# Optimization experiments

Hardware: AMD Instinct MI355X
Metric: run time of the kernel (lower is better)

The kernel has to match this reference:

```python
import jax, jax.numpy as jnp
import numpy as np

# Bit-slice configuration from the module defaults: slices [1,1,2,4] -> 8-bit signed INT.
# The crossbar engine's MapReduceDot decomposes the quantized integers into bit-planes,
# runs partial dot products per (input-slice, weight-slice) pair across paral_size
# partitions, and recombines them with 2^shift weights. In the ideal (noise-free)
# engine this recombination is EXACT, so the forward math equals:
#   dequant(blockwise_quant(x)) @ dequant(blockwise_quant(W^T)) + bias
# with per-block scales determined by the quant granularities.
IN_BITS = 1 + 1 + 2 + 4   # sum(input_slice)  = 8
W_BITS = 1 + 1 + 2 + 4    # sum(weight_slice) = 8
IN_GRAN = (1, 32)         # (rows, cols) blocks over (seq, in_features)
W_GRAN = (32, 32)         # blocks over (in_features, out_features) of weight.t()


def block_fake_quant(x, bits, gran):
    """Symmetric per-block fake quantization (quantize -> dequantize).

    x: [..., R, C]; gran=(gr, gc) tiles the last two dims. Each (gr, gc) block
    gets its own max-abs scale, matching SlicedData's quant_gran semantics.
    """
    qmax = float(2 ** (bits - 1) - 1)  # 127 for 8-bit
    gr, gc = gran
    lead = x.shape[:-2]
    R, C = x.shape[-2], x.shape[-1]
    xb = x.reshape(*lead, R // gr, gr, C // gc, gc)
    mx = jnp.max(jnp.abs(xb), axis=(-3, -1), keepdims=True)
    scale = jnp.where(mx > 0, mx / qmax, jnp.ones_like(mx))
    q = jnp.clip(jnp.round(xb / scale), -qmax, qmax) * scale
    return q.reshape(x.shape)


def setup_inputs() -> dict:
    key = jax.random.key(0)
    k1, k2, k3 = jax.random.split(key, 3)
    B, S, Din, Dout = 4, 4096, 2048, 2048
    x = jax.random.normal(k1, (B, S, Din), dtype=jnp.float32)
    # kaiming_uniform_(a=sqrt(5)) on a Linear weight is U(-1/sqrt(fan_in), 1/sqrt(fan_in))
    bound = 1.0 / np.sqrt(Din)
    weight = jax.random.uniform(k2, (Dout, Din), jnp.float32, -bound, bound)
    bias = jax.random.uniform(k3, (Dout,), jnp.float32, -bound, bound)
    return {"x": x, "weight": weight, "bias": bias}


def reference(x, weight, bias):
    # Quantize activations per (1, 32) block and weight.t() per (32, 32) block,
    # then recombine via the (mathematically exact) bit-sliced dot == dense GEMM
    # on the dequantized values.
    qx = block_fake_quant(x, IN_BITS, IN_GRAN)            # [B, S, Din]
    qw = block_fake_quant(weight.T, W_BITS, W_GRAN)       # [Din, Dout]
    out = jnp.einsum('bsd,de->bse', qx, qw) + bias        # [B, S, Dout]
    return out
```

## Files before the change

### kernel.cpp

```cpp
#include <hip/hip_runtime.h>
#include <hip/hip_bf16.h>
#include <stdint.h>

#define M_TOT 16384
#define N_TOT 2048
#define K_TOT 2048
#define NT 32

typedef __attribute__((ext_vector_type(8))) short bf16x8;
typedef __attribute__((ext_vector_type(4))) float f32x4;

__device__ __forceinline__ ushort f32_to_bf16_rne(float f) {
    uint32_t u = __float_as_uint(f);
    uint32_t r = (u + 0x7fffu + ((u >> 16) & 1u)) >> 16;
    return (ushort)r;
}

__device__ __forceinline__ void async_copy16(const void* gptr, void* lptr) {
    __builtin_amdgcn_global_load_lds(
        (const __attribute__((address_space(1))) uint32_t*)gptr,
        (__attribute__((address_space(3))) uint32_t*)lptr,
        16, 0, 0);
}

__global__ void quant_x_kernel(const float* __restrict__ x, ushort* __restrict__ qx) {
    const int tid = blockIdx.x * 256 + threadIdx.x;
    const float4 v = ((const float4*)x)[tid];
    float m = fmaxf(fmaxf(fabsf(v.x), fabsf(v.y)), fmaxf(fabsf(v.z), fabsf(v.w)));
    m = fmaxf(m, __shfl_xor(m, 1));
    m = fmaxf(m, __shfl_xor(m, 2));
    m = fmaxf(m, __shfl_xor(m, 4));
    const float s = (m > 0.f) ? (m / 127.f) : 1.f;
    const float q0 = fminf(fmaxf(rintf(v.x / s), -127.f), 127.f) * s;
    const float q1 = fminf(fmaxf(rintf(v.y / s), -127.f), 127.f) * s;
    const float q2 = fminf(fmaxf(rintf(v.z / s), -127.f), 127.f) * s;
    const float q3 = fminf(fmaxf(rintf(v.w / s), -127.f), 127.f) * s;
    ushort4 r;
    r.x = f32_to_bf16_rne(q0);
    r.y = f32_to_bf16_rne(q1);
    r.z = f32_to_bf16_rne(q2);
    r.w = f32_to_bf16_rne(q3);
    ((ushort4*)qx)[tid] = r;
}

__global__ void quant_w_kernel(const float* __restrict__ w, ushort* __restrict__ qw) {
    const int gtid = blockIdx.x * 256 + threadIdx.x;
    const int wid  = gtid >> 6;
    const int lane = gtid & 63;
    const int tn = wid >> 6;
    const int tk = wid & 63;
    const int row = tn * 32 + (lane >> 1);
    const int col = tk * 32 + ((lane & 1) << 4);
    const float* p = w + (size_t)row * K_TOT + col;
    const float4 v0 = ((const float4*)p)[0];
    const float4 v1 = ((const float4*)p)[1];
    const float4 v2 = ((const float4*)p)[2];
    const float4 v3 = ((const float4*)p)[3];
    float m = 0.f;
#define MAX4(V) m = fmaxf(m, fmaxf(fmaxf(fabsf(V.x), fabsf(V.y)), fmaxf(fabsf(V.z), fabsf(V.w))));
    MAX4(v0) MAX4(v1) MAX4(v2) MAX4(v3)
#undef MAX4
    #pragma unroll
    for (int off = 1; off < 64; off <<= 1) m = fmaxf(m, __shfl_xor(m, off));
    const float s = (m > 0.f) ? (m / 127.f) : 1.f;
    float vv[16] = {v0.x, v0.y, v0.z, v0.w, v1.x, v1.y, v1.z, v1.w,
                    v2.x, v2.y, v2.z, v2.w, v3.x, v3.y, v3.z, v3.w};
    union { ushort us[16]; uint4 q[2]; } o;
    #pragma unroll
    for (int i = 0; i < 16; ++i) {
        const float q = fminf(fmaxf(rintf(vv[i] / s), -127.f), 127.f) * s;
        o.us[i] = f32_to_bf16_rne(q);
    }
    uint4* dst = (uint4*)(qw + (size_t)row * K_TOT + col);
    dst[0] = o.q[0];
    dst[1] = o.q[1];
}

#define LDSA(tb, row, colus) \
    (*(const bf16x8*)&As[tb][row][(colus) ^ (((row) & 7) << 3)])
#define LDSB(tb, row, colus) \
    (*(const bf16x8*)&Bs[tb][row][(colus) ^ (((row) & 7) << 3)])

#define STAGE_A(tb, hh, li, tt)                                                          \
    async_copy16(Agbase + (size_t)((hh) * 128 + (li) * 64) * K_TOT + (size_t)(tt) * 64,  \
                 (char*)&As[0][0][0] + (tb) * 32768 + (hh) * 16384 + (li) * 8192 + (wv << 10))
#define STAGE_B(tb, hh, li, tt)                                                          \
    async_copy16(Bgbase + (size_t)((hh) * 128 + (li) * 64) * K_TOT + (size_t)(tt) * 64,  \
                 (char*)&Bs[0][0][0] + (tb) * 32768 + (hh) * 16384 + (li) * 8192 + (wv << 10))
#define STAGE_A2(tb, hh, tt)  { STAGE_A(tb, hh, 0, tt); STAGE_A(tb, hh, 1, tt); }
#define STAGE_B2(tb, hh, tt)  { STAGE_B(tb, hh, 0, tt); STAGE_B(tb, hh, 1, tt); }

#define PHASE_MFMA(i0)                                                                    \
    asm volatile("s_waitcnt lgkmcnt(0)" ::: "memory");                                    \
    __builtin_amdgcn_s_setprio(1);                                                        \
    _Pragma("unroll")                                                                     \
    for (int j = 0; j < 4; ++j) {                                                         \
        acc[i0][j]     = __builtin_amdgcn_mfma_f32_16x16x32_bf16(af0, bg[j][0], acc[i0][j], 0, 0, 0);     \
        acc[i0][j]     = __builtin_amdgcn_mfma_f32_16x16x32_bf16(af1, bg[j][1], acc[i0][j], 0, 0, 0);     \
        acc[(i0)+1][j] = __builtin_amdgcn_mfma_f32_16x16x32_bf16(af2, bg[j][0], acc[(i0)+1][j], 0, 0, 0); \
        acc[(i0)+1][j] = __builtin_amdgcn_mfma_f32_16x16x32_bf16(af3, bg[j][1], acc[(i0)+1][j], 0, 0, 0); \
    }                                                                                     \
    __builtin_amdgcn_s_setprio(0);

#define TILE_BODY(tb, t)                                                                  \
  {                                                                                       \
    bf16x8 af0, af1, af2, af3;                                                            \
    bf16x8 bg[4][2];                                                                      \
                      \
    af0 = LDSA(tb, ab +  0, h8);  af1 = LDSA(tb, ab +  0, 32 + h8);                       \
    af2 = LDSA(tb, ab + 16, h8);  af3 = LDSA(tb, ab + 16, 32 + h8);                       \
    bg[0][0] = LDSB(tb, bb0, h8);  bg[0][1] = LDSB(tb, bb0, 32 + h8);                     \
    bg[1][0] = LDSB(tb, bb1, h8);  bg[1][1] = LDSB(tb, bb1, 32 + h8);                     \
    bg[2][0] = LDSB(tb, bb2, h8);  bg[2][1] = LDSB(tb, bb2, 32 + h8);                     \
    bg[3][0] = LDSB(tb, bb3, h8);  bg[3][1] = LDSB(tb, bb3, 32 + h8);                     \
    if ((t) + 1 < NT) STAGE_A2(tb ^ 1, 0, (t) + 1)                                        \
    asm volatile("s_waitcnt lgkmcnt(8)" ::: "memory");                                    \
    __builtin_amdgcn_s_barrier();                                                         \
    PHASE_MFMA(0)                                                                         \
    __builtin_amdgcn_s_barrier();                                                         \
                                \
    af0 = LDSA(tb, ab + 32, h8);  af1 = LDSA(tb, ab + 32, 32 + h8);                       \
    af2 = LDSA(tb, ab + 48, h8);  af3 = LDSA(tb, ab + 48, 32 + h8);                       \
    if ((t) + 1 < NT) STAGE_A2(tb ^ 1, 1, (t) + 1)                                        \
    __builtin_amdgcn_s_barrier();                                                         \
    PHASE_MFMA(2)                                                                         \
    __builtin_amdgcn_s_barrier();                                                         \
           \
    af0 = LDSA(tb, ab + 64, h8);  af1 = LDSA(tb, ab + 64, 32 + h8);                       \
    af2 = LDSA(tb, ab + 80, h8);  af3 = LDSA(tb, ab + 80, 32 + h8);                       \
    if ((t) + 2 < NT) STAGE_B2(tb, 0, (t) + 2)                                            \
    __builtin_amdgcn_s_barrier();                                                         \
    PHASE_MFMA(4)                                                                         \
    __builtin_amdgcn_s_barrier();                                                         \
                \
    af0 = LDSA(tb, ab +  96, h8);  af1 = LDSA(tb, ab +  96, 32 + h8);                     \
    af2 = LDSA(tb, ab + 112, h8);  af3 = LDSA(tb, ab + 112, 32 + h8);                     \
    if ((t) + 2 < NT) STAGE_B2(tb, 1, (t) + 2)                                            \
    __builtin_amdgcn_s_barrier();                                                         \
    PHASE_MFMA(6)                                                                         \
    if ((t) + 2 < NT) { asm volatile("s_waitcnt vmcnt(4)" ::: "memory"); }                \
    else              { asm volatile("s_waitcnt vmcnt(0)" ::: "memory"); }                \
    __builtin_amdgcn_s_barrier();                                                         \
  }

__global__ __launch_bounds__(512, 1) void gemm_8ph_kernel(
    const ushort* __restrict__ A,
    const ushort* __restrict__ Bt,
    const float* __restrict__ bias,
    float* __restrict__ C) {

    __shared__ ushort As[2][256][64];
    __shared__ ushort Bs[2][256][64];

    const int tid  = threadIdx.x;
    const int lane = tid & 63;
    const int wv   = tid >> 6;
    const int wmr  = wv >> 2;
    const int wcn  = wv & 3;
    const int r    = lane & 15;
    const int h8   = (lane >> 4) << 3;

    const int nbn  = N_TOT / 256;
    const int nwg  = (M_TOT / 256) * nbn;
    const int cpx  = nwg >> 3;
    const int swz  = (blockIdx.x & 7) * cpx + (blockIdx.x >> 3);
    const int brow = (swz / nbn) * 256;
    const int bcol = (swz % nbn) * 256;

    const int srow = tid >> 3;
    const int scol = (((tid & 7) ^ (srow & 7)) << 3);
    const ushort* Agbase = A  + (size_t)(brow + srow) * K_TOT + scol;
    const ushort* Bgbase = Bt + (size_t)(bcol + srow) * K_TOT + scol;

    const int ab  = wmr * 128 + r;
    const int bb0 = wcn * 64 +  0 + r;
    const int bb1 = wcn * 64 + 16 + r;
    const int bb2 = wcn * 64 + 32 + r;
    const int bb3 = wcn * 64 + 48 + r;

    f32x4 acc[8][4];
    const f32x4 zero = {0.f, 0.f, 0.f, 0.f};
    #pragma unroll
    for (int i = 0; i < 8; ++i)
        #pragma unroll
        for (int j = 0; j < 4; ++j) acc[i][j] = zero;

    STAGE_A2(0, 0, 0) STAGE_A2(0, 1, 0)
    STAGE_B2(0, 0, 0) STAGE_B2(0, 1, 0)
    STAGE_B2(1, 0, 1) STAGE_B2(1, 1, 1)
    asm volatile("s_waitcnt vmcnt(4)" ::: "memory");
    __builtin_amdgcn_s_barrier();

    for (int t = 0; t < NT; t += 2) {
        TILE_BODY(0, t)
        TILE_BODY(1, t + 1)
    }

    const int hq = (lane >> 4) * 4;
    float bv[4];
    #pragma unroll
    for (int j = 0; j < 4; ++j) bv[j] = bias[bcol + wcn * 64 + j * 16 + r];
    #pragma unroll
    for (int i = 0; i < 8; ++i) {
        const int row0 = brow + wmr * 128 + i * 16 + hq;
        #pragma unroll
        for (int j = 0; j < 4; ++j) {
            const int col = bcol + wcn * 64 + j * 16 + r;
            #pragma unroll
            for (int jj = 0; jj < 4; ++jj)
                C[(size_t)(row0 + jj) * N_TOT + col] = acc[i][j][jj] + bv[j];
        }
    }
}

extern "C" void kernel_launch(void* const* d_in, const int* in_sizes, int n_in,
                              void* d_out, int out_size, void* d_ws, size_t ws_size,
                              hipStream_t stream) {
    const float* x    = (const float*)d_in[0];
    const float* wgt  = (const float*)d_in[1];
    const float* bias = (const float*)d_in[2];
    float* out = (float*)d_out;

    ushort* qx = (ushort*)d_ws;
    ushort* qw = qx + (size_t)M_TOT * K_TOT;

    quant_x_kernel<<<(M_TOT * K_TOT / 4) / 256, 256, 0, stream>>>(x, qx);
    quant_w_kernel<<<(64 * 64 * 64) / 256, 256, 0, stream>>>(wgt, qw);
    gemm_8ph_kernel<<<(M_TOT / 256) * (N_TOT / 256), 512, 0, stream>>>(qx, qw, bias, out);
}
```

Before: 175.3 us.

## Ping-pong A fragments in registers and drop most per-phase barriers in GEMM loop

Restructures the GEMM main loop so A fragments are double-buffered in two register sets (afX/afY). The LDS read for the next phase is issued before the current phase's MFMAs, using partial lgkmcnt waits and sched_barriers. Block-wide barriers drop from eight per K-tile to two, and the last two tiles are peeled to remove per-iteration staging conditionals. It also changes launch_bounds to request two 512-thread blocks per CU. That cap likely squeezes registers against the 128-float accumulator and may cause spills, while the LDS footprint per block probably prevents two blocks from co-residing anyway.

```diff
diff --git a/kernel.cpp b/kernel.cpp
--- a/kernel.cpp
+++ b/kernel.cpp
@@ -83,67 +83,69 @@
 
 #define STAGE_A(tb, hh, li, tt)                                                          \
     async_copy16(Agbase + (size_t)((hh) * 128 + (li) * 64) * K_TOT + (size_t)(tt) * 64,  \
-                 (char*)&As[0][0][0] + (tb) * 32768 + (hh) * 16384 + (li) * 8192 + (wv << 10))
+                 (char*)&As[0][0][0] + (tb) * 32768 + (hh) * 16384 + (li) * 8192 + (wv << 10));
 #define STAGE_B(tb, hh, li, tt)                                                          \
     async_copy16(Bgbase + (size_t)((hh) * 128 + (li) * 64) * K_TOT + (size_t)(tt) * 64,  \
-                 (char*)&Bs[0][0][0] + (tb) * 32768 + (hh) * 16384 + (li) * 8192 + (wv << 10))
-#define STAGE_A2(tb, hh, tt)  { STAGE_A(tb, hh, 0, tt); STAGE_A(tb, hh, 1, tt); }
-#define STAGE_B2(tb, hh, tt)  { STAGE_B(tb, hh, 0, tt); STAGE_B(tb, hh, 1, tt); }
-
-#define PHASE_MFMA(i0)                                                                    \
-    asm volatile("s_waitcnt lgkmcnt(0)" ::: "memory");                                    \
+                 (char*)&Bs[0][0][0] + (tb) * 32768 + (hh) * 16384 + (li) * 8192 + (wv << 10));
+#define STAGE_A2(tb, hh, tt)  { STAGE_A(tb, hh, 0, tt) STAGE_A(tb, hh, 1, tt) }
+#define STAGE_B2(tb, hh, tt)  { STAGE_B(tb, hh, 0, tt) STAGE_B(tb, hh, 1, tt) }
+
+#define WAITLGKM4 { asm volatile("s_waitcnt lgkmcnt(4)" ::: "memory"); __builtin_amdgcn_sched_barrier(0); }
+#define WAITLGKM0 { asm volatile("s_waitcnt lgkmcnt(0)" ::: "memory"); __builtin_amdgcn_sched_barrier(0); }
+#define WAITVM4   { asm volatile("s_waitcnt vmcnt(4)" ::: "memory"); }
+#define WAITVM0   { asm volatile("s_waitcnt vmcnt(0)" ::: "memory"); }
+
+#define RD_AF(DST, tb, q) {                                   \
+    DST[0] = LDSA(tb, ab + (q) * 32,      h8);                \
+    DST[1] = LDSA(tb, ab + (q) * 32,      32 + h8);           \
+    DST[2] = LDSA(tb, ab + (q) * 32 + 16, h8);                \
+    DST[3] = LDSA(tb, ab + (q) * 32 + 16, 32 + h8); }
+
+#define MFMA_PH(i0, AF)                                                                   \
     __builtin_amdgcn_s_setprio(1);                                                        \
     _Pragma("unroll")                                                                     \
     for (int j = 0; j < 4; ++j) {                                                         \
-        acc[i0][j]     = __builtin_amdgcn_mfma_f32_16x16x32_bf16(af0, bg[j][0], acc[i0][j], 0, 0, 0);     \
-        acc[i0][j]     = __builtin_amdgcn_mfma_f32_16x16x32_bf16(af1, bg[j][1], acc[i0][j], 0, 0, 0);     \
-        acc[(i0)+1][j] = __builtin_amdgcn_mfma_f32_16x16x32_bf16(af2, bg[j][0], acc[(i0)+1][j], 0, 0, 0); \
-        acc[(i0)+1][j] = __builtin_amdgcn_mfma_f32_16x16x32_bf16(af3, bg[j][1], acc[(i0)+1][j], 0, 0, 0); \
+        acc[i0][j]     = __builtin_amdgcn_mfma_f32_16x16x32_bf16(AF[0], bg[j][0], acc[i0][j], 0, 0, 0);     \
+        acc[i0][j]     = __builtin_amdgcn_mfma_f32_16x16x32_bf16(AF[1], bg[j][1], acc[i0][j], 0, 0, 0);     \
+        acc[(i0)+1][j] = __builtin_amdgcn_mfma_f32_16x16x32_bf16(AF[2], bg[j][0], acc[(i0)+1][j], 0, 0, 0); \
+        acc[(i0)+1][j] = __builtin_amdgcn_mfma_f32_16x16x32_bf16(AF[3], bg[j][1], acc[(i0)+1][j], 0, 0, 0); \
     }                                                                                     \
     __builtin_amdgcn_s_setprio(0);
 
-#define TILE_BODY(tb, t)                                                                  \
+#define TILE_BODY(tb, t, STA, STB, VMC)                                                   \
   {                                                                                       \
-    bf16x8 af0, af1, af2, af3;                                                            \
-    bf16x8 bg[4][2];                                                                      \
-                      \
-    af0 = LDSA(tb, ab +  0, h8);  af1 = LDSA(tb, ab +  0, 32 + h8);                       \
-    af2 = LDSA(tb, ab + 16, h8);  af3 = LDSA(tb, ab + 16, 32 + h8);                       \
-    bg[0][0] = LDSB(tb, bb0, h8);  bg[0][1] = LDSB(tb, bb0, 32 + h8);                     \
-    bg[1][0] = LDSB(tb, bb1, h8);  bg[1][1] = LDSB(tb, bb1, 32 + h8);                     \
-    bg[2][0] = LDSB(tb, bb2, h8);  bg[2][1] = LDSB(tb, bb2, 32 + h8);                     \
-    bg[3][0] = LDSB(tb, bb3, h8);  bg[3][1] = LDSB(tb, bb3, 32 + h8);                     \
-    if ((t) + 1 < NT) STAGE_A2(tb ^ 1, 0, (t) + 1)                                        \
-    asm volatile("s_waitcnt lgkmcnt(8)" ::: "memory");                                    \
-    __builtin_amdgcn_s_barrier();                                                         \
-    PHASE_MFMA(0)                                                                         \
-    __builtin_amdgcn_s_barrier();                                                         \
-                                \
-    af0 = LDSA(tb, ab + 32, h8);  af1 = LDSA(tb, ab + 32, 32 + h8);                       \
-    af2 = LDSA(tb, ab + 48, h8);  af3 = LDSA(tb, ab + 48, 32 + h8);                       \
-    if ((t) + 1 < NT) STAGE_A2(tb ^ 1, 1, (t) + 1)                                        \
-    __builtin_amdgcn_s_barrier();                                                         \
-    PHASE_MFMA(2)                                                                         \
-    __builtin_amdgcn_s_barrier();                                                         \
-           \
-    af0 = LDSA(tb, ab + 64, h8);  af1 = LDSA(tb, ab + 64, 32 + h8);                       \
-    af2 = LDSA(tb, ab + 80, h8);  af3 = LDSA(tb, ab + 80, 32 + h8);                       \
-    if ((t) + 2 < NT) STAGE_B2(tb, 0, (t) + 2)                                            \
-    __builtin_amdgcn_s_barrier();                                                         \
-    PHASE_MFMA(4)                                                                         \
-    __builtin_amdgcn_s_barrier();                                                         \
-                \
-    af0 = LDSA(tb, ab +  96, h8);  af1 = LDSA(tb, ab +  96, 32 + h8);                     \
-    af2 = LDSA(tb, ab + 112, h8);  af3 = LDSA(tb, ab + 112, 32 + h8);                     \
-    if ((t) + 2 < NT) STAGE_B2(tb, 1, (t) + 2)                                            \
-    __builtin_amdgcn_s_barrier();                                                         \
-    PHASE_MFMA(6)                                                                         \
-    if ((t) + 2 < NT) { asm volatile("s_waitcnt vmcnt(4)" ::: "memory"); }                \
-    else              { asm volatile("s_waitcnt vmcnt(0)" ::: "memory"); }                \
-    __builtin_amdgcn_s_barrier();                                                         \
+               \
+    RD_AF(afX, tb, 0)                                                                     \
+    _Pragma("unroll")                                                                     \
+    for (int j = 0; j < 4; ++j) {                                                         \
+        const int bb = wcn * 64 + j * 16 + r;                                             \
+        bg[j][0] = LDSB(tb, bb, h8);  bg[j][1] = LDSB(tb, bb, 32 + h8);                   \
+    }                                                                                     \
+    RD_AF(afY, tb, 1)                                                                     \
+    if (STA) STAGE_A2(tb ^ 1, 0, (t) + 1)                                                 \
+    WAITLGKM4                                                                             \
+    MFMA_PH(0, afX)                                                                       \
+                                 \
+    RD_AF(afX, tb, 2)                                                                     \
+    if (STA) STAGE_A2(tb ^ 1, 1, (t) + 1)                                                 \
+    WAITLGKM4                                                                             \
+    MFMA_PH(2, afY)                                                                       \
+    __builtin_amdgcn_s_barrier();                \
+                                 \
+    RD_AF(afY, tb, 3)                                                                     \
+    if (STB) STAGE_B2(tb, 0, (t) + 2)                                                     \
+    WAITLGKM4                                                                             \
+    MFMA_PH(4, afX)                                                                       \
+                       \
+    if (STB) STAGE_B2(tb, 1, (t) + 2)                                                     \
+    WAITLGKM0                                                                             \
+    MFMA_PH(6, afY)                                                                       \
+    if ((VMC) == 4)      WAITVM4                                                          \
+    else if ((VMC) == 0) WAITVM0                                                          \
+    __builtin_amdgcn_s_barrier();                       \
   }
 
-__global__ __launch_bounds__(512, 1) void gemm_8ph_kernel(
+__global__ __launch_bounds__(512, 2) void gemm_pipe2_kernel(
     const ushort* __restrict__ A,
     const ushort* __restrict__ Bt,
     const float* __restrict__ bias,
@@ -172,11 +174,7 @@
     const ushort* Agbase = A  + (size_t)(brow + srow) * K_TOT + scol;
     const ushort* Bgbase = Bt + (size_t)(bcol + srow) * K_TOT + scol;
 
-    const int ab  = wmr * 128 + r;
-    const int bb0 = wcn * 64 +  0 + r;
-    const int bb1 = wcn * 64 + 16 + r;
-    const int bb2 = wcn * 64 + 32 + r;
-    const int bb3 = wcn * 64 + 48 + r;
+    const int ab = wmr * 128 + r;
 
     f32x4 acc[8][4];
     const f32x4 zero = {0.f, 0.f, 0.f, 0.f};
@@ -188,13 +186,18 @@
     STAGE_A2(0, 0, 0) STAGE_A2(0, 1, 0)
     STAGE_B2(0, 0, 0) STAGE_B2(0, 1, 0)
     STAGE_B2(1, 0, 1) STAGE_B2(1, 1, 1)
-    asm volatile("s_waitcnt vmcnt(4)" ::: "memory");
+    WAITVM0
     __builtin_amdgcn_s_barrier();
 
-    for (int t = 0; t < NT; t += 2) {
-        TILE_BODY(0, t)
-        TILE_BODY(1, t + 1)
+    bf16x8 afX[4], afY[4];
+    bf16x8 bg[4][2];
+
+    for (int t = 0; t < NT - 2; t += 2) {
+        TILE_BODY(0, t,     1, 1, 4)
+        TILE_BODY(1, t + 1, 1, 1, 4)
     }
+    TILE_BODY(0, NT - 2, 1, 0, 0)
+    TILE_BODY(1, NT - 1, 0, 0, -1)
 
     const int hq = (lane >> 4) * 4;
     float bv[4];
@@ -226,5 +229,5 @@
 
     quant_x_kernel<<<(M_TOT * K_TOT / 4) / 256, 256, 0, stream>>>(x, qx);
     quant_w_kernel<<<(64 * 64 * 64) / 256, 256, 0, stream>>>(wgt, qw);
-    gemm_8ph_kernel<<<(M_TOT / 256) * (N_TOT / 256), 512, 0, stream>>>(qx, qw, bias, out);
-}
+    gemm_pipe2_kernel<<<(M_TOT / 256) * (N_TOT / 256), 512, 0, stream>>>(qx, qw, bias, out);
+}
```

After: 166.3 us. 5.1% less time.
